# Optimization experiments

Measured on AMD Instinct MI355X. Metric: run time of the kernel, lower is better.

The kernel has to match this reference:

```python
import jax, jax.numpy as jnp
import numpy as np
from jax import lax

# Derived constants for kernel=(51,5), stride=1, VH='V':
#   mink=5, maxk=51, nk=11, conv padding=(5,2), shift pads along H.
NK = 11
PADS = [20, 15, 10, 5, 0, -5, -10, -15, -20, -25, -30]
MINK = 5
MAXK = 51
BN_EPS = 1e-5


def setup_inputs() -> dict:
    key = jax.random.key(0)
    k1, k2, k3, k4 = jax.random.split(key, 4)
    B, Cin, Cout, Hh, Ww = 8, 256, 256, 64, 64
    x = jax.random.normal(k1, (B, Cin, Hh, Ww), dtype=jnp.float32)
    # split_convs weight: [out_channels*nk, in_channels, 5, 5]
    weight = jax.random.normal(k2, (Cout * NK, Cin, MINK, MINK), dtype=jnp.float32) * 0.02
    gamma = 1.0 + 0.1 * jax.random.normal(k3, (Cout,), dtype=jnp.float32)
    beta = 0.1 * jax.random.normal(k4, (Cout,), dtype=jnp.float32)
    return {"x": x, "weight": weight, "gamma": gamma, "beta": beta}


def reference(x, weight, gamma, beta):
    # 1) grouped (group=1 here) small-kernel conv producing nk sub-maps per out channel
    y = lax.conv_general_dilated(
        x, weight, window_strides=(1, 1),
        padding=((5, 5), (2, 2)),
        dimension_numbers=("NCHW", "OIHW", "NCHW"),
        feature_group_count=1,
    )  # [B, Cout*nk, h, w], h = H_in + 6, w = W_in
    B, C, h, w = y.shape
    c1 = C // NK
    ori_h = x.shape[2]
    H = (ori_h + 2 * (MAXK // 2) - MAXK) + 1  # stride 1 -> H == ori_h
    y = y.reshape(B, c1, NK, h, w)

    # 2) shift/gather reassembly (RUN_TAICHI): out[b,c,i,j] = sum_idx y[b,c,idx, i - pads[idx], j]
    out = jnp.zeros((B, c1, H, w), dtype=y.dtype)
    for idx, p in enumerate(PADS):
        a = max(0, p)
        b = min(H, h + p)
        if a < b:
            out = out.at[:, :, a:b, :].add(y[:, :, idx, a - p:b - p, :])

    # 3) BatchNorm2d (training-mode batch statistics, as in SyncBatchNorm forward)
    mean = out.mean(axis=(0, 2, 3))
    var = out.var(axis=(0, 2, 3))
    scale = gamma * lax.rsqrt(var + BN_EPS)
    return out * scale[None, :, None, None] + (beta - mean * scale)[None, :, None, None]
```

## Files before the change

kernel.cpp:

```cpp
#include <hip/hip_runtime.h>

typedef __attribute__((ext_vector_type(8))) short short8;
typedef __attribute__((ext_vector_type(8))) unsigned short ushort8;
typedef __attribute__((ext_vector_type(4))) float f32x4;

#define K_DIM 70400
#define KHALF 1100
#define XROWS 118
#define XCOLS 68
#define BUF 16384
#define BOFFB 8192

#define XPACK_ELEMS (8 * XROWS * XCOLS * 256)
#define XPACK_BYTES (XPACK_ELEMS * 2)
#define APACK_ELEMS (256 * K_DIM)
#define APACK_BYTES (APACK_ELEMS * 2)

static __device__ __forceinline__ unsigned short f2bf(float f) {
    unsigned u = __builtin_bit_cast(unsigned, f);
    u += 0x7fffu + ((u >> 16) & 1u);
    return (unsigned short)(u >> 16);
}

static __device__ __forceinline__ void mfma16(f32x4& acc, short8 a, short8 b) {
    asm("v_mfma_f32_16x16x32_bf16 %0, %1, %2, %0" : "+v"(acc) : "v"(a), "v"(b));
}

#define GLOAD_LDS(gp, lp) __builtin_amdgcn_global_load_lds( \
    (const __attribute__((address_space(1))) void*)(gp),    \
    (__attribute__((address_space(3))) void*)(lp), 16, 0, 0)

#define BAR() __builtin_amdgcn_s_barrier()
#define LGKM0() do { asm volatile("s_waitcnt lgkmcnt(0)" ::: "memory"); \
                     __builtin_amdgcn_sched_barrier(0); } while (0)


__global__ __launch_bounds__(256) void zero_ws_kernel(ushort8* __restrict__ p, int n) {
    int i = blockIdx.x * 256 + threadIdx.x;
    if (i < n) { ushort8 z = {}; p[i] = z; }
}

__global__ __launch_bounds__(256) void zero_out_kernel(f32x4* __restrict__ p) {
    int i = blockIdx.x * 256 + threadIdx.x;
    f32x4 z = {};
    p[i] = z;
}

__global__ __launch_bounds__(256) void pack_x_kernel(const float* __restrict__ x,
                                                     unsigned short* __restrict__ xp) {
    int g = blockIdx.x * 256 + threadIdx.x;
    int xc = g & 63;
    int rest = g >> 6;
    int chunk = rest & 31;
    int br = rest >> 5;
    int xr = br & 63;
    int b  = br >> 6;
    const float* src = x + (long)(b * 256 + chunk * 8) * 4096 + xr * 64 + xc;
    ushort8 o;
#pragma unroll
    for (int e = 0; e < 8; ++e) o[e] = f2bf(src[(long)e * 4096]);
    long off = ((long)((b * XROWS + xr + 25) * XCOLS + (xc + 2))) * 256 + chunk * 8;
    *(ushort8*)(xp + off) = o;
}

__global__ __launch_bounds__(256) void pack_w_kernel(const float* __restrict__ W,
                                                     unsigned short* __restrict__ Apk) {
    int c = blockIdx.x, t = threadIdx.x;
    __shared__ float lw[6400];
    for (int idx = 0; idx < 11; ++idx) {
        const float* src = W + (long)(c * 11 + idx) * 6400;
        for (int e = t; e < 6400; e += 256) lw[e] = src[e];
        __syncthreads();
#pragma unroll 5
        for (int khw = 0; khw < 25; ++khw)
            Apk[(long)c * K_DIM + (idx * 25 + khw) * 256 + t] = f2bf(lw[t * 25 + khw]);
        __syncthreads();
    }
}

__global__ __launch_bounds__(512) void gemm_kernel(const unsigned short* __restrict__ Apk,
                                                   const unsigned short* __restrict__ Xpk,
                                                   float* __restrict__ out) {
    __shared__ unsigned short lds[4 * BUF];
    const int t = threadIdx.x;
    int bid = blockIdx.x;
    int swz = (bid & 7) * 32 + (bid >> 3);
    const int nt = swz >> 1;
    const int ks = swz & 1;
    const int n0 = nt * 256;
    const int k0 = ks * KHALF;

    const int lane = t & 63;
    const int w = t >> 6;
    const int wm = w >> 2;
    const int wn = w & 3;
    const int lrow = lane & 15;
    const int lsg = lane >> 4;

    int offA[8], offB[4];
#pragma unroll
    for (int m = 0; m < 8; ++m) {
        int ra = wm * 128 + m * 16 + lrow;
        offA[m] = ra * 32 + ((lsg ^ (ra & 3)) << 3);
    }
#pragma unroll
    for (int nf = 0; nf < 4; ++nf) {
        int rb = wn * 64 + nf * 16 + lrow;
        offB[nf] = BOFFB + rb * 32 + ((lsg ^ (rb & 3)) << 3);
    }

    const unsigned short* aS[2];
    const unsigned short* bS[2];
    int aD[2], bD[2];
#pragma unroll
    for (int p = 0; p < 2; ++p) {
        int ch = p * 512 + t;
        int row = ch >> 2;
        int s = (ch & 3) ^ (row & 3);
        aS[p] = Apk + (long)row * K_DIM + s * 8;
        aD[p] = ch * 8;
        int n = n0 + row;
        int b = n >> 12, i = (n >> 6) & 63, j = n & 63;
        bS[p] = Xpk + ((long)((b * XROWS + i) * XCOLS + j)) * 256 + s * 8;
        bD[p] = BOFFB + ch * 8;
    }

#pragma unroll
    for (int pre = 0; pre < 3; ++pre) {
        int kt = k0 + pre;
        int qB = pre * BUF;
        int dA = kt << 5;
        int g = kt >> 3, v = g / 5, kw = g - v * 5;
        int dB = (v * XCOLS + kw) * 256 + ((kt & 7) << 5);
        GLOAD_LDS(aS[0] + dA, lds + qB + aD[0]);
        GLOAD_LDS(aS[1] + dA, lds + qB + aD[1]);
        GLOAD_LDS(bS[0] + dB, lds + qB + bD[0]);
        GLOAD_LDS(bS[1] + dB, lds + qB + bD[1]);
    }
    asm volatile("s_waitcnt vmcnt(8)" ::: "memory");
    BAR();

    f32x4 acc[8][4] = {};

    for (int ktl = 0; ktl < KHALF; ++ktl) {
        const int qcB = (ktl & 3) * BUF;
        const int qsB = ((ktl + 3) & 3) * BUF;
        const bool st = (ktl + 3) < KHALF;
        const int kt3 = k0 + ktl + 3;
        const int dA3 = kt3 << 5;
        int g3 = kt3 >> 3, v3 = g3 / 5, kw3 = g3 - v3 * 5;
        const int dB3 = (v3 * XCOLS + kw3) * 256 + ((kt3 & 7) << 5);

        short8 af[8], b0, b1, b2, b3;
#pragma unroll
        for (int m = 0; m < 8; ++m) af[m] = *(const short8*)(lds + qcB + offA[m]);
        b0 = *(const short8*)(lds + qcB + offB[0]);
        b1 = *(const short8*)(lds + qcB + offB[1]);
        b2 = *(const short8*)(lds + qcB + offB[2]);
        b3 = *(const short8*)(lds + qcB + offB[3]);
        if (st) { GLOAD_LDS(aS[0] + dA3, lds + qsB + aD[0]);
                  GLOAD_LDS(aS[1] + dA3, lds + qsB + aD[1]); }
        BAR(); LGKM0();
        __builtin_amdgcn_s_setprio(1);
#pragma unroll
        for (int m = 0; m < 8; ++m) { mfma16(acc[m][0], af[m], b0); mfma16(acc[m][1], af[m], b1); }
        __builtin_amdgcn_s_setprio(0);
        BAR();
        if (st) { GLOAD_LDS(bS[0] + dB3, lds + qsB + bD[0]);
                  GLOAD_LDS(bS[1] + dB3, lds + qsB + bD[1]); }
        BAR(); LGKM0();
        __builtin_amdgcn_s_setprio(1);
#pragma unroll
        for (int m = 0; m < 8; ++m) { mfma16(acc[m][2], af[m], b2); mfma16(acc[m][3], af[m], b3); }
        __builtin_amdgcn_s_setprio(0);
        if (st) asm volatile("s_waitcnt vmcnt(8)" ::: "memory");
        else    asm volatile("s_waitcnt vmcnt(0)" ::: "memory");
        BAR();
    }

    const int b = n0 >> 12;
    float* ob = out + (long)b * 1048576 + (n0 & 4095) + wn * 64 + (lane & 15);
#pragma unroll
    for (int m = 0; m < 8; ++m)
#pragma unroll
        for (int qi = 0; qi < 4; ++qi) {
            int row = wm * 128 + m * 16 + (lane >> 4) * 4 + qi;
            float* orow = ob + (long)row * 4096;
#pragma unroll
            for (int nf = 0; nf < 4; ++nf)
                unsafeAtomicAdd(orow + nf * 16, acc[m][nf][qi]);
        }
}


__global__ __launch_bounds__(256) void bn_stats_kernel(const float* __restrict__ out,
                                                       const float* __restrict__ gamma,
                                                       const float* __restrict__ beta,
                                                       float* __restrict__ bnp) {
    int c = blockIdx.x, t = threadIdx.x;
    float s = 0.f, q = 0.f;
    for (int b = 0; b < 8; ++b) {
        const float* p = out + (long)b * 1048576 + (long)c * 4096;
        for (int e = t; e < 4096; e += 256) { float v = p[e]; s += v; q += v * v; }
    }
#pragma unroll
    for (int off = 32; off > 0; off >>= 1) { s += __shfl_down(s, off); q += __shfl_down(q, off); }
    __shared__ float ls[4], lq[4];
    int w = t >> 6;
    if ((t & 63) == 0) { ls[w] = s; lq[w] = q; }
    __syncthreads();
    if (t == 0) {
        s = ls[0] + ls[1] + ls[2] + ls[3];
        q = lq[0] + lq[1] + lq[2] + lq[3];
        float mean = s * (1.f / 32768.f);
        float var = q * (1.f / 32768.f) - mean * mean;
        float sc = gamma[c] * rsqrtf(var + 1e-5f);
        bnp[c] = sc;
        bnp[256 + c] = beta[c] - mean * sc;
    }
}

__global__ __launch_bounds__(256) void bn_apply_kernel(float* __restrict__ out,
                                                       const float* __restrict__ bnp) {
    int i = blockIdx.x * 256 + threadIdx.x;
    f32x4* p = (f32x4*)out;
    f32x4 v = p[i];
    int c = (i >> 10) & 255;
    float sc = bnp[c], sh = bnp[256 + c];
    v = v * sc + sh;
    p[i] = v;
}


extern "C" void kernel_launch(void* const* d_in, const int* in_sizes, int n_in,
                              void* d_out, int out_size, void* d_ws, size_t ws_size,
                              hipStream_t stream) {
    const float* x     = (const float*)d_in[0];
    const float* wgt   = (const float*)d_in[1];
    const float* gamma = (const float*)d_in[2];
    const float* beta  = (const float*)d_in[3];
    float* out = (float*)d_out;

    unsigned short* xp  = (unsigned short*)d_ws;
    unsigned short* Apk = (unsigned short*)((char*)d_ws + XPACK_BYTES);
    float* bnp          = (float*)((char*)d_ws + XPACK_BYTES + APACK_BYTES);

    zero_ws_kernel<<<8024, 256, 0, stream>>>((ushort8*)xp, XPACK_ELEMS / 8);
    pack_x_kernel<<<4096, 256, 0, stream>>>(x, xp);
    pack_w_kernel<<<256, 256, 0, stream>>>(wgt, Apk);
    zero_out_kernel<<<8192, 256, 0, stream>>>((f32x4*)out);
    gemm_kernel<<<256, 512, 0, stream>>>(Apk, xp, out);
    bn_stats_kernel<<<256, 256, 0, stream>>>(out, gamma, beta, bnp);
    bn_apply_kernel<<<8192, 256, 0, stream>>>(out, bnp);
}
```

Baseline: 1.349 ms.

## Double K tile to 64 with double-buffered LDS and 8-way swizzle

The GEMM main loop now consumes a K-slice of 64 per iteration instead of 32, halving the iteration count. The 4-stage 32-wide LDS ring becomes a 2-stage 64-wide double buffer, and the XOR swizzle widens from 4 to 8 chunks per row. The A fragments are split into two halves to keep register pressure bounded. The aim is to amortize barriers and per-iteration overhead over more MFMAs, at the cost of a shallower prefetch: the loop waits with vmcnt(0) every iteration, so global-load latency may be exposed.

```diff
diff --git a/kernel.cpp b/kernel.cpp
--- a/kernel.cpp
+++ b/kernel.cpp
@@ -5,11 +5,11 @@
 typedef __attribute__((ext_vector_type(4))) float f32x4;
 
 #define K_DIM 70400
-#define KHALF 1100
+#define KHALF 550
 #define XROWS 118
 #define XCOLS 68
-#define BUF 16384
-#define BOFFB 8192
+#define BUF32 32768
+#define BOFFB 16384
 
 #define XPACK_ELEMS (8 * XROWS * XCOLS * 256)
 #define XPACK_BYTES (XPACK_ELEMS * 2)
@@ -81,7 +81,7 @@
 __global__ __launch_bounds__(512) void gemm_kernel(const unsigned short* __restrict__ Apk,
                                                    const unsigned short* __restrict__ Xpk,
                                                    float* __restrict__ out) {
-    __shared__ unsigned short lds[4 * BUF];
+    __shared__ unsigned short lds[2 * BUF32];
     const int t = threadIdx.x;
     int bid = blockIdx.x;
     int swz = (bid & 7) * 32 + (bid >> 3);
@@ -97,98 +97,138 @@
     const int lrow = lane & 15;
     const int lsg = lane >> 4;
 
-    int offA[8], offB[4];
-#pragma unroll
-    for (int m = 0; m < 8; ++m) {
-        int ra = wm * 128 + m * 16 + lrow;
-        offA[m] = ra * 32 + ((lsg ^ (ra & 3)) << 3);
-    }
-#pragma unroll
-    for (int nf = 0; nf < 4; ++nf) {
-        int rb = wn * 64 + nf * 16 + lrow;
-        offB[nf] = BOFFB + rb * 32 + ((lsg ^ (rb & 3)) << 3);
-    }
-
-    const unsigned short* aS[2];
-    const unsigned short* bS[2];
-    int aD[2], bD[2];
-#pragma unroll
-    for (int p = 0; p < 2; ++p) {
-        int ch = p * 512 + t;
-        int row = ch >> 2;
-        int s = (ch & 3) ^ (row & 3);
-        aS[p] = Apk + (long)row * K_DIM + s * 8;
-        aD[p] = ch * 8;
-        int n = n0 + row;
-        int b = n >> 12, i = (n >> 6) & 63, j = n & 63;
-        bS[p] = Xpk + ((long)((b * XROWS + i) * XCOLS + j)) * 256 + s * 8;
-        bD[p] = BOFFB + ch * 8;
-    }
-
-#pragma unroll
-    for (int pre = 0; pre < 3; ++pre) {
-        int kt = k0 + pre;
-        int qB = pre * BUF;
-        int dA = kt << 5;
-        int g = kt >> 3, v = g / 5, kw = g - v * 5;
-        int dB = (v * XCOLS + kw) * 256 + ((kt & 7) << 5);
-        GLOAD_LDS(aS[0] + dA, lds + qB + aD[0]);
-        GLOAD_LDS(aS[1] + dA, lds + qB + aD[1]);
-        GLOAD_LDS(bS[0] + dB, lds + qB + bD[0]);
-        GLOAD_LDS(bS[1] + dB, lds + qB + bD[1]);
-    }
-    asm volatile("s_waitcnt vmcnt(8)" ::: "memory");
+    int offA[8][2], offB[4][2];
+#pragma unroll
+    for (int mf = 0; mf < 8; ++mf)
+#pragma unroll
+        for (int kk = 0; kk < 2; ++kk) {
+            int sd = kk * 4 + lsg;
+            int ra = wm * 128 + mf * 16 + lrow;
+            offA[mf][kk] = ra * 64 + ((sd ^ (ra & 7)) << 3);
+        }
+#pragma unroll
+    for (int nf = 0; nf < 4; ++nf)
+#pragma unroll
+        for (int kk = 0; kk < 2; ++kk) {
+            int sd = kk * 4 + lsg;
+            int rb = wn * 64 + nf * 16 + lrow;
+            offB[nf][kk] = BOFFB + rb * 64 + ((sd ^ (rb & 7)) << 3);
+        }
+
+    const unsigned short* aS[4];
+    const unsigned short* bS[4];
+    int aD[4], bD[4];
+    {
+        int s = (t & 7) ^ ((t >> 3) & 7);
+#pragma unroll
+        for (int p = 0; p < 4; ++p) {
+            int ch = p * 512 + t;
+            int row = p * 64 + (t >> 3);
+            aS[p] = Apk + (long)row * K_DIM + s * 8;
+            aD[p] = ch * 8;
+            int n = n0 + row;
+            int b = n >> 12, i = (n >> 6) & 63, j = n & 63;
+            bS[p] = Xpk + ((long)((b * XROWS + i) * XCOLS + j)) * 256 + s * 8;
+            bD[p] = BOFFB + ch * 8;
+        }
+    }
+
+    {
+        int kt = k0;
+        int dA = kt << 6;
+        int g = kt >> 2, v = g / 5, kw = g - v * 5;
+        int dB = (v * XCOLS + kw) * 256 + ((kt & 3) << 6);
+#pragma unroll
+        for (int p = 0; p < 4; ++p) GLOAD_LDS(aS[p] + dA, lds + aD[p]);
+#pragma unroll
+        for (int p = 0; p < 4; ++p) GLOAD_LDS(bS[p] + dB, lds + bD[p]);
+    }
+    asm volatile("s_waitcnt vmcnt(0)" ::: "memory");
     BAR();
 
     f32x4 acc[8][4] = {};
 
     for (int ktl = 0; ktl < KHALF; ++ktl) {
-        const int qcB = (ktl & 3) * BUF;
-        const int qsB = ((ktl + 3) & 3) * BUF;
-        const bool st = (ktl + 3) < KHALF;
-        const int kt3 = k0 + ktl + 3;
-        const int dA3 = kt3 << 5;
-        int g3 = kt3 >> 3, v3 = g3 / 5, kw3 = g3 - v3 * 5;
-        const int dB3 = (v3 * XCOLS + kw3) * 256 + ((kt3 & 7) << 5);
-
-        short8 af[8], b0, b1, b2, b3;
-#pragma unroll
-        for (int m = 0; m < 8; ++m) af[m] = *(const short8*)(lds + qcB + offA[m]);
-        b0 = *(const short8*)(lds + qcB + offB[0]);
-        b1 = *(const short8*)(lds + qcB + offB[1]);
-        b2 = *(const short8*)(lds + qcB + offB[2]);
-        b3 = *(const short8*)(lds + qcB + offB[3]);
-        if (st) { GLOAD_LDS(aS[0] + dA3, lds + qsB + aD[0]);
-                  GLOAD_LDS(aS[1] + dA3, lds + qsB + aD[1]); }
+        const int cur = (ktl & 1) * BUF32;
+        const int nxt = ((ktl + 1) & 1) * BUF32;
+        const bool st = (ktl + 1) < KHALF;
+        const int kt1 = k0 + ktl + 1;
+        const int dA1 = kt1 << 6;
+        int g1 = kt1 >> 2, v1 = g1 / 5, kw1 = g1 - v1 * 5;
+        const int dB1 = (v1 * XCOLS + kw1) * 256 + ((kt1 & 3) << 6);
+
+        short8 af[4][2], bf[4][2];
+#pragma unroll
+        for (int mf = 0; mf < 4; ++mf) { af[mf][0] = *(const short8*)(lds + cur + offA[mf][0]);
+                                         af[mf][1] = *(const short8*)(lds + cur + offA[mf][1]); }
+        bf[0][0] = *(const short8*)(lds + cur + offB[0][0]);
+        bf[0][1] = *(const short8*)(lds + cur + offB[0][1]);
+        bf[1][0] = *(const short8*)(lds + cur + offB[1][0]);
+        bf[1][1] = *(const short8*)(lds + cur + offB[1][1]);
+        if (st) {
+#pragma unroll
+            for (int p = 0; p < 4; ++p) GLOAD_LDS(aS[p] + dA1, lds + nxt + aD[p]);
+        }
         BAR(); LGKM0();
         __builtin_amdgcn_s_setprio(1);
 #pragma unroll
-        for (int m = 0; m < 8; ++m) { mfma16(acc[m][0], af[m], b0); mfma16(acc[m][1], af[m], b1); }
-        __builtin_amdgcn_s_setprio(0);
-        BAR();
-        if (st) { GLOAD_LDS(bS[0] + dB3, lds + qsB + bD[0]);
-                  GLOAD_LDS(bS[1] + dB3, lds + qsB + bD[1]); }
+        for (int mf = 0; mf < 4; ++mf)
+#pragma unroll
+            for (int kk = 0; kk < 2; ++kk) { mfma16(acc[mf][0], af[mf][kk], bf[0][kk]);
+                                             mfma16(acc[mf][1], af[mf][kk], bf[1][kk]); }
+        __builtin_amdgcn_s_setprio(0);
+        BAR();
+        bf[2][0] = *(const short8*)(lds + cur + offB[2][0]);
+        bf[2][1] = *(const short8*)(lds + cur + offB[2][1]);
+        bf[3][0] = *(const short8*)(lds + cur + offB[3][0]);
+        bf[3][1] = *(const short8*)(lds + cur + offB[3][1]);
+        if (st) {
+#pragma unroll
+            for (int p = 0; p < 4; ++p) GLOAD_LDS(bS[p] + dB1, lds + nxt + bD[p]);
+        }
         BAR(); LGKM0();
         __builtin_amdgcn_s_setprio(1);
 #pragma unroll
-        for (int m = 0; m < 8; ++m) { mfma16(acc[m][2], af[m], b2); mfma16(acc[m][3], af[m], b3); }
-        __builtin_amdgcn_s_setprio(0);
-        if (st) asm volatile("s_waitcnt vmcnt(8)" ::: "memory");
-        else    asm volatile("s_waitcnt vmcnt(0)" ::: "memory");
+        for (int mf = 0; mf < 4; ++mf)
+#pragma unroll
+            for (int kk = 0; kk < 2; ++kk) { mfma16(acc[mf][2], af[mf][kk], bf[2][kk]);
+                                             mfma16(acc[mf][3], af[mf][kk], bf[3][kk]); }
+        __builtin_amdgcn_s_setprio(0);
+        BAR();
+#pragma unroll
+        for (int mf = 0; mf < 4; ++mf) { af[mf][0] = *(const short8*)(lds + cur + offA[mf + 4][0]);
+                                         af[mf][1] = *(const short8*)(lds + cur + offA[mf + 4][1]); }
+        BAR(); LGKM0();
+        __builtin_amdgcn_s_setprio(1);
+#pragma unroll
+        for (int mf = 0; mf < 4; ++mf)
+#pragma unroll
+            for (int kk = 0; kk < 2; ++kk) { mfma16(acc[mf + 4][0], af[mf][kk], bf[0][kk]);
+                                             mfma16(acc[mf + 4][1], af[mf][kk], bf[1][kk]); }
+        __builtin_amdgcn_s_setprio(0);
+        BAR();
+        __builtin_amdgcn_s_setprio(1);
+#pragma unroll
+        for (int mf = 0; mf < 4; ++mf)
+#pragma unroll
+            for (int kk = 0; kk < 2; ++kk) { mfma16(acc[mf + 4][2], af[mf][kk], bf[2][kk]);
+                                             mfma16(acc[mf + 4][3], af[mf][kk], bf[3][kk]); }
+        __builtin_amdgcn_s_setprio(0);
+        asm volatile("s_waitcnt vmcnt(0)" ::: "memory");
         BAR();
     }
 
     const int b = n0 >> 12;
     float* ob = out + (long)b * 1048576 + (n0 & 4095) + wn * 64 + (lane & 15);
 #pragma unroll
-    for (int m = 0; m < 8; ++m)
+    for (int mf = 0; mf < 8; ++mf)
 #pragma unroll
         for (int qi = 0; qi < 4; ++qi) {
-            int row = wm * 128 + m * 16 + (lane >> 4) * 4 + qi;
+            int row = wm * 128 + mf * 16 + (lane >> 4) * 4 + qi;
             float* orow = ob + (long)row * 4096;
 #pragma unroll
             for (int nf = 0; nf < 4; ++nf)
-                unsafeAtomicAdd(orow + nf * 16, acc[m][nf][qi]);
+                unsafeAtomicAdd(orow + nf * 16, acc[mf][nf][qi]);
         }
 }
 
```

Measured after the change: 1.091 ms. 19.1% less time.
